# Performance work log

Hardware: AMD Instinct MI355X
Metric: run time of the kernel (lower is better)

## Reference

```python
import jax, jax.numpy as jnp
import numpy as np

N_GRID = 64
DX = 1.0 / N_GRID
INV_DX = float(N_GRID)
DT = 5e-4
BOUND = 3
GRAVITY = np.array([0.0, -9.8, 0.0], dtype=np.float32)
P_VOL = (DX * 0.5) ** 3          # particle volume (NCLaw convention)
P_RHO = 1000.0
P_MASS = P_VOL * P_RHO
N_PART = 500000


def setup_inputs() -> dict:
    key = jax.random.key(0)
    k1, k2, k3, k4, k5 = jax.random.split(key, 5)
    # particles inside the domain, away from the boundary
    x = 0.2 + 0.6 * jax.random.uniform(k1, (N_PART, 3), dtype=jnp.float32)
    v = 0.1 * jax.random.normal(k2, (N_PART, 3), dtype=jnp.float32)
    C = 0.1 * jax.random.normal(k3, (N_PART, 3, 3), dtype=jnp.float32)
    F = jnp.eye(3, dtype=jnp.float32)[None] + 0.01 * jax.random.normal(k4, (N_PART, 3, 3), dtype=jnp.float32)
    s = jax.random.normal(k5, (N_PART, 3, 3), dtype=jnp.float32)
    stress = 100.0 * 0.5 * (s + jnp.swapaxes(s, -1, -2))  # symmetric Cauchy stress
    return {"x": x, "v": v, "C": C, "F": F, "stress": stress}


def _mpm_step(x, v, C, F, stress):
    # quadratic B-spline stencil
    base = jnp.floor(x * INV_DX - 0.5).astype(jnp.int32)        # [N,3]
    fx = x * INV_DX - base.astype(x.dtype)                      # [N,3]
    # weights per offset (0,1,2) per axis -> [N,3(off),3(dim)]
    w = jnp.stack([0.5 * (1.5 - fx) ** 2,
                   0.75 - (fx - 1.0) ** 2,
                   0.5 * (fx - 0.5) ** 2], axis=1)
    # MLS-MPM fused stress + APIC affine term
    affine = stress * (-DT * P_VOL * 4.0 * INV_DX * INV_DX) + P_MASS * C  # [N,3,3]

    offs = jnp.stack(jnp.meshgrid(jnp.arange(3), jnp.arange(3), jnp.arange(3),
                                  indexing='ij'), axis=-1).reshape(27, 3)  # [27,3]
    wi = w[:, offs[:, 0], 0] * w[:, offs[:, 1], 1] * w[:, offs[:, 2], 2]   # [N,27]
    dpos = (offs[None, :, :].astype(x.dtype) - fx[:, None, :]) * DX        # [N,27,3] physical
    mom = P_MASS * v[:, None, :] + jnp.einsum('nij,nkj->nki', affine, dpos)  # [N,27,3]

    idx = base[:, None, :] + offs[None, :, :]                               # [N,27,3]
    flat = (idx[..., 0] * N_GRID + idx[..., 1]) * N_GRID + idx[..., 2]      # [N,27]
    flat_r = flat.reshape(-1)
    G = N_GRID ** 3
    grid_mv = jnp.zeros((G, 3), dtype=x.dtype).at[flat_r].add((wi[..., None] * mom).reshape(-1, 3))
    grid_m = jnp.zeros((G,), dtype=x.dtype).at[flat_r].add((wi * P_MASS).reshape(-1))

    has_mass = grid_m > 0.0
    grid_v = jnp.where(has_mass[:, None], grid_mv / jnp.maximum(grid_m, 1e-10)[:, None], 0.0)
    grid_v = jnp.where(has_mass[:, None], grid_v + DT * jnp.asarray(GRAVITY, x.dtype), 0.0)

    # sticky-ish boundary: zero inflow velocity near walls
    gi = jnp.arange(G)
    ijk = jnp.stack([gi // (N_GRID * N_GRID), (gi // N_GRID) % N_GRID, gi % N_GRID], axis=-1)
    low = (ijk < BOUND) & (grid_v < 0.0)
    high = (ijk >= N_GRID - BOUND) & (grid_v > 0.0)
    grid_v = jnp.where(low | high, 0.0, grid_v)

    # G2P gather
    gv = grid_v[flat]                                              # [N,27,3]
    v_next = jnp.einsum('nk,nkd->nd', wi, gv)                      # [N,3]
    C_next = (4.0 * INV_DX * INV_DX) * jnp.einsum('nk,nki,nkj->nij', wi, gv, dpos)
    x_next = x + DT * v_next
    F_next = jnp.einsum('nij,njk->nik', jnp.eye(3, dtype=x.dtype)[None] + DT * C_next, F)
    return x_next, v_next, C_next, F_next


def reference(x, v, C, F, stress):
    return _mpm_step(x, v, C, F, stress)
```

## Files before the change

kernel.cpp:

```cpp
#include <hip/hip_runtime.h>
#include <math.h>

namespace {
constexpr int   NG    = 64;
constexpr int   GC    = NG * NG * NG;
constexpr int   BOUND = 3;
constexpr float DXf    = 1.0f / 64.0f;
constexpr float INV_DX = 64.0f;
constexpr float DTf    = 5e-4f;
constexpr double P_VOL_D = (0.5 / 64.0) * (0.5 / 64.0) * (0.5 / 64.0);
constexpr float P_MASS_F = (float)(P_VOL_D * 1000.0);
constexpr float AFFINE_SCALE = (float)(-5e-4 * P_VOL_D * 4.0 * 64.0 * 64.0);
constexpr float D_INV  = 4.0f * 64.0f * 64.0f;
constexpr float GRAV_Y = -9.8f;

__device__ __forceinline__ void atom_add_f32(float* p, float v) {
    unsafeAtomicAdd(p, v);
}

__device__ __forceinline__ void weights_of(float fx0, float fx1, float fx2, float w[3][3]) {
    w[0][0] = 0.5f*(1.5f-fx0)*(1.5f-fx0); w[0][1] = 0.5f*(1.5f-fx1)*(1.5f-fx1); w[0][2] = 0.5f*(1.5f-fx2)*(1.5f-fx2);
    w[1][0] = 0.75f-(fx0-1.0f)*(fx0-1.0f); w[1][1] = 0.75f-(fx1-1.0f)*(fx1-1.0f); w[1][2] = 0.75f-(fx2-1.0f)*(fx2-1.0f);
    w[2][0] = 0.5f*(fx0-0.5f)*(fx0-0.5f); w[2][1] = 0.5f*(fx1-0.5f)*(fx1-0.5f); w[2][2] = 0.5f*(fx2-0.5f)*(fx2-0.5f);
}

__device__ __forceinline__ float bspline_w(float u) {
    float au = fabsf(u);
    float a  = 1.5f - au;
    float w  = (au < 0.5f) ? (0.75f - u * u) : (0.5f * a * a);
    return (au < 1.5f) ? w : 0.f;
}
}

__global__ __launch_bounds__(256) void count_kernel(const float* __restrict__ x,
                                                    int* __restrict__ cnt, int n)
{
    int p = blockIdx.x * 256 + threadIdx.x;
    if (p >= n) return;
    float u0 = x[3*p] * INV_DX, u1 = x[3*p+1] * INV_DX, u2 = x[3*p+2] * INV_DX;
    int b0 = (int)floorf(u0 - 0.5f), b1 = (int)floorf(u1 - 0.5f), b2 = (int)floorf(u2 - 0.5f);
    if ((unsigned)b0 >= 64u || (unsigned)b1 >= 64u || (unsigned)b2 >= 64u) return;
    atomicAdd(&cnt[((b0 << 6) + b1) * 64 + b2], 1);
}

__global__ __launch_bounds__(256) void scanA(const int* __restrict__ cnt,
                                             int* __restrict__ start,
                                             int* __restrict__ aux)
{
    __shared__ int sh[256];
    int tid = threadIdx.x;
    int i = blockIdx.x * 256 + tid;
    int v = cnt[i];
    sh[tid] = v;
    __syncthreads();
    for (int off = 1; off < 256; off <<= 1) {
        int t = (tid >= off) ? sh[tid - off] : 0;
        __syncthreads();
        sh[tid] += t;
        __syncthreads();
    }
    start[i] = sh[tid] - v;
    if (tid == 255) aux[blockIdx.x] = sh[255];
}

__global__ __launch_bounds__(256) void scanC(int* __restrict__ start,
                                             const int* __restrict__ aux,
                                             int* __restrict__ cursor)
{
    __shared__ int partial[256];
    __shared__ int sa[1024];
    int tid = threadIdx.x;
    int local[4];
    int s = 0;
#pragma unroll
    for (int k = 0; k < 4; ++k) { local[k] = s; s += aux[tid * 4 + k]; }
    partial[tid] = s;
    __syncthreads();
    for (int off = 1; off < 256; off <<= 1) {
        int v = (tid >= off) ? partial[tid - off] : 0;
        __syncthreads();
        partial[tid] += v;
        __syncthreads();
    }
    int base = (tid > 0) ? partial[tid - 1] : 0;
#pragma unroll
    for (int k = 0; k < 4; ++k) sa[tid * 4 + k] = base + local[k];
    __syncthreads();
    int off0 = sa[blockIdx.x];
    int i = blockIdx.x * 256 + tid;
    int v = start[i] + off0;
    start[i] = v;
    cursor[i] = v;
    if (blockIdx.x == 0 && tid == 0) start[GC] = sa[1023] + aux[1023];
}

__global__ __launch_bounds__(256) void reorder_kernel(const float* __restrict__ x,
                                                      const float* __restrict__ v,
                                                      const float* __restrict__ C,
                                                      const float* __restrict__ st,
                                                      int* __restrict__ cursor,
                                                      float4* __restrict__ pay0,
                                                      float4* __restrict__ pay1,
                                                      float4* __restrict__ pay2,
                                                      float4* __restrict__ pay3, int n)
{
    int p = blockIdx.x * 256 + threadIdx.x;
    if (p >= n) return;

    float u0 = x[3*p] * INV_DX, u1 = x[3*p+1] * INV_DX, u2 = x[3*p+2] * INV_DX;
    int b0 = (int)floorf(u0 - 0.5f), b1 = (int)floorf(u1 - 0.5f), b2 = (int)floorf(u2 - 0.5f);
    if ((unsigned)b0 >= 64u || (unsigned)b1 >= 64u || (unsigned)b2 >= 64u) return;

    float aff[9];
#pragma unroll
    for (int i = 0; i < 9; ++i)
        aff[i] = st[9*p + i] * AFFINE_SCALE + P_MASS_F * C[9*p + i];
    float mv0 = P_MASS_F * v[3*p], mv1 = P_MASS_F * v[3*p+1], mv2 = P_MASS_F * v[3*p+2];

    int pos = atomicAdd(&cursor[((b0 << 6) + b1) * 64 + b2], 1);

    pay0[pos] = make_float4(aff[0], aff[1], aff[2], aff[3]);
    pay1[pos] = make_float4(aff[4], aff[5], aff[6], aff[7]);
    pay2[pos] = make_float4(aff[8], mv0, mv1, mv2);
    pay3[pos] = make_float4(u0, u1, u2, 0.f);
}

__global__ __launch_bounds__(256) void p2g_strip(const float4* __restrict__ pay0,
                                                 const float4* __restrict__ pay1,
                                                 const float4* __restrict__ pay2,
                                                 const float4* __restrict__ pay3,
                                                 const int* __restrict__ start,
                                                 float* __restrict__ grid)
{
    int B   = blockIdx.x;
    int xcd = B & 7, j = B >> 3;
    int cj  = j >> 2, oj = j & 3;
    int wave = threadIdx.x >> 6, lane = threadIdx.x & 63;
    int r   = ((cj * 32 + xcd * 4 + oj) << 2) + wave;

    int row01 = r >> 1;
    int g0 = row01 >> 6, g1 = row01 & 63;
    int sl = lane >> 3, q = lane & 7;
    int g2b = ((r & 1) << 5) + sl * 4;
    float fg0 = (float)g0, fg1 = (float)g1, fg2b = (float)g2b;

    float a00=0.f,a01=0.f,a02=0.f,a03=0.f;
    float a10=0.f,a11=0.f,a12=0.f,a13=0.f;
    float a20=0.f,a21=0.f,a22=0.f,a23=0.f;
    float a30=0.f,a31=0.f,a32=0.f,a33=0.f;

    int klo = (g2b >= 2) ? g2b - 2 : 0;
    int khi = (g2b + 3 <= 63) ? g2b + 3 : 63;

#define P2G_CELL(CC, A0, A1, A2, A3)                                         \
    {   float u2  = r3.z - (fg2b + (float)CC);                               \
        float w2  = bspline_w(u2);                                           \
        float wq  = w01 * w2;                                                \
        float dp2 = -u2 * DXf;                                               \
        A0 += wq * (m0 + r0.z * dp2);                                        \
        A1 += wq * (m1 + r1.y * dp2);                                        \
        A2 += wq * (m2 + r2.x * dp2);                                        \
        A3 += wq * P_MASS_F; }

#pragma unroll
    for (int o0 = 0; o0 < 3; ++o0) {
        int b0 = g0 - o0;
        if ((unsigned)b0 >= 64u) continue;
#pragma unroll
        for (int o1 = 0; o1 < 3; ++o1) {
            int b1 = g1 - o1;
            if ((unsigned)b1 >= 64u) continue;
            int rowp = ((b0 << 6) + b1) << 6;
            int s = start[rowp + klo] + q;
            int e = start[rowp + khi + 1];
            float4 c0, c1, c2, c3;
            if (s < e) { c0 = pay0[s]; c1 = pay1[s]; c2 = pay2[s]; c3 = pay3[s]; }
            for (int idx = s; idx < e; ) {
                float4 r0 = c0, r1 = c1, r2 = c2, r3 = c3;
                idx += 8;
                if (idx < e) { c0 = pay0[idx]; c1 = pay1[idx]; c2 = pay2[idx]; c3 = pay3[idx]; }
                float u0  = r3.x - fg0, u1 = r3.y - fg1;
                float w01 = bspline_w(u0) * bspline_w(u1);
                float dp0 = -u0 * DXf, dp1 = -u1 * DXf;
                float m0 = r2.y + r0.x * dp0 + r0.y * dp1;
                float m1 = r2.z + r0.w * dp0 + r1.x * dp1;
                float m2 = r2.w + r1.z * dp0 + r1.w * dp1;
                P2G_CELL(0, a00, a01, a02, a03)
                P2G_CELL(1, a10, a11, a12, a13)
                P2G_CELL(2, a20, a21, a22, a23)
                P2G_CELL(3, a30, a31, a32, a33)
            }
        }
    }
#undef P2G_CELL

#define RED(OFF)                                                             \
    a00 += __shfl_down(a00, OFF); a01 += __shfl_down(a01, OFF);              \
    a02 += __shfl_down(a02, OFF); a03 += __shfl_down(a03, OFF);              \
    a10 += __shfl_down(a10, OFF); a11 += __shfl_down(a11, OFF);              \
    a12 += __shfl_down(a12, OFF); a13 += __shfl_down(a13, OFF);              \
    a20 += __shfl_down(a20, OFF); a21 += __shfl_down(a21, OFF);              \
    a22 += __shfl_down(a22, OFF); a23 += __shfl_down(a23, OFF);              \
    a30 += __shfl_down(a30, OFF); a31 += __shfl_down(a31, OFF);              \
    a32 += __shfl_down(a32, OFF); a33 += __shfl_down(a33, OFF);
    RED(1) RED(2) RED(4)
#undef RED

    if (q == 0) {
#define STORE_CELL(CC, A0, A1, A2, A3)                                       \
    {   int g2 = g2b + CC;                                                   \
        float v0 = 0.f, v1 = 0.f, v2 = 0.f;                                  \
        if (A3 > 0.f) {                                                      \
            float mm = fmaxf(A3, 1e-10f);                                    \
            v0 = A0 / mm;                                                    \
            v1 = A1 / mm + DTf * GRAV_Y;                                     \
            v2 = A2 / mm;                                                    \
        }                                                                    \
        if ((g0 < BOUND && v0 < 0.f) || (g0 >= NG - BOUND && v0 > 0.f)) v0 = 0.f; \
        if ((g1 < BOUND && v1 < 0.f) || (g1 >= NG - BOUND && v1 > 0.f)) v1 = 0.f; \
        if ((g2 < BOUND && v2 < 0.f) || (g2 >= NG - BOUND && v2 > 0.f)) v2 = 0.f; \
        ((float4*)grid)[row01 * 64 + g2] = make_float4(v0, v1, v2, A3); }
        STORE_CELL(0, a00, a01, a02, a03)
        STORE_CELL(1, a10, a11, a12, a13)
        STORE_CELL(2, a20, a21, a22, a23)
        STORE_CELL(3, a30, a31, a32, a33)
#undef STORE_CELL
    }
}

__global__ __launch_bounds__(256) void p2g_naive(const float* __restrict__ x,
                                                 const float* __restrict__ v,
                                                 const float* __restrict__ C,
                                                 const float* __restrict__ st,
                                                 float* __restrict__ grid, int n)
{
    int p = blockIdx.x * 256 + threadIdx.x;
    if (p >= n) return;

    float xp0 = x[3*p], xp1 = x[3*p+1], xp2 = x[3*p+2];
    float u0 = xp0 * INV_DX, u1 = xp1 * INV_DX, u2 = xp2 * INV_DX;
    float b0f = floorf(u0 - 0.5f), b1f = floorf(u1 - 0.5f), b2f = floorf(u2 - 0.5f);
    int base0 = (int)b0f, base1 = (int)b1f, base2 = (int)b2f;
    float fx0 = u0 - b0f, fx1 = u1 - b1f, fx2 = u2 - b2f;

    float w[3][3];
    weights_of(fx0, fx1, fx2, w);

    float aff[3][3];
#pragma unroll
    for (int i = 0; i < 3; ++i)
#pragma unroll
        for (int j = 0; j < 3; ++j)
            aff[i][j] = st[9*p + 3*i + j] * AFFINE_SCALE + P_MASS_F * C[9*p + 3*i + j];

    float mv0 = P_MASS_F * v[3*p], mv1 = P_MASS_F * v[3*p+1], mv2 = P_MASS_F * v[3*p+2];

#pragma unroll
    for (int i = 0; i < 3; ++i) {
        float dp0 = ((float)i - fx0) * DXf;
#pragma unroll
        for (int j = 0; j < 3; ++j) {
            float dp1 = ((float)j - fx1) * DXf;
            float wij = w[i][0] * w[j][1];
            float m0 = mv0 + aff[0][0]*dp0 + aff[0][1]*dp1;
            float m1 = mv1 + aff[1][0]*dp0 + aff[1][1]*dp1;
            float m2 = mv2 + aff[2][0]*dp0 + aff[2][1]*dp1;
            int cellij = ((base0 + i) * NG + (base1 + j)) * NG + base2;
#pragma unroll
            for (int k = 0; k < 3; ++k) {
                float dp2 = ((float)k - fx2) * DXf;
                float wi = wij * w[k][2];
                float* cptr = grid + 4 * (cellij + k);
                atom_add_f32(cptr + 0, wi * (m0 + aff[0][2]*dp2));
                atom_add_f32(cptr + 1, wi * (m1 + aff[1][2]*dp2));
                atom_add_f32(cptr + 2, wi * (m2 + aff[2][2]*dp2));
                atom_add_f32(cptr + 3, wi * P_MASS_F);
            }
        }
    }
}

__global__ __launch_bounds__(256) void grid_kernel(float* __restrict__ grid)
{
    int g = blockIdx.x * 256 + threadIdx.x;
    if (g >= GC) return;
    float4 val = ((const float4*)grid)[g];
    float m = val.w;
    float v0 = 0.f, v1 = 0.f, v2 = 0.f;
    if (m > 0.f) {
        float mm = fmaxf(m, 1e-10f);
        v0 = val.x / mm;
        v1 = val.y / mm + DTf * GRAV_Y;
        v2 = val.z / mm;
    }
    int ci = g >> 12, cj = (g >> 6) & 63, ck = g & 63;
    if ((ci < BOUND && v0 < 0.f) || (ci >= NG - BOUND && v0 > 0.f)) v0 = 0.f;
    if ((cj < BOUND && v1 < 0.f) || (cj >= NG - BOUND && v1 > 0.f)) v1 = 0.f;
    if ((ck < BOUND && v2 < 0.f) || (ck >= NG - BOUND && v2 > 0.f)) v2 = 0.f;
    ((float4*)grid)[g] = make_float4(v0, v1, v2, m);
}

__global__ __launch_bounds__(256) void g2p_kernel(const float* __restrict__ x,
                                                  const float* __restrict__ F,
                                                  const float* __restrict__ grid,
                                                  float* __restrict__ out_x,
                                                  float* __restrict__ out_v,
                                                  float* __restrict__ out_C,
                                                  float* __restrict__ out_F,
                                                  int n)
{
    int p = blockIdx.x * 256 + threadIdx.x;
    if (p >= n) return;

    float xp0 = x[3*p], xp1 = x[3*p+1], xp2 = x[3*p+2];
    float t0 = xp0 * INV_DX, t1 = xp1 * INV_DX, t2 = xp2 * INV_DX;
    float b0 = floorf(t0 - 0.5f), b1 = floorf(t1 - 0.5f), b2 = floorf(t2 - 0.5f);
    int   base0 = (int)b0, base1 = (int)b1, base2 = (int)b2;
    float fx0 = t0 - b0, fx1 = t1 - b1, fx2 = t2 - b2;

    float w[3][3];
    weights_of(fx0, fx1, fx2, w);

    float vn0 = 0.f, vn1 = 0.f, vn2 = 0.f;
    float Cn[3][3] = {};

#pragma unroll
    for (int i = 0; i < 3; ++i) {
        float dp0 = ((float)i - fx0) * DXf;
#pragma unroll
        for (int j = 0; j < 3; ++j) {
            float dp1 = ((float)j - fx1) * DXf;
            float wij = w[i][0] * w[j][1];
            int cellij = ((base0 + i) * NG + (base1 + j)) * NG + base2;
#pragma unroll
            for (int k = 0; k < 3; ++k) {
                float dp2 = ((float)k - fx2) * DXf;
                float wi = wij * w[k][2];
                float4 gv = ((const float4*)grid)[cellij + k];
                vn0 += wi * gv.x; vn1 += wi * gv.y; vn2 += wi * gv.z;
                float wx = wi * gv.x, wy = wi * gv.y, wz = wi * gv.z;
                Cn[0][0] += wx * dp0; Cn[0][1] += wx * dp1; Cn[0][2] += wx * dp2;
                Cn[1][0] += wy * dp0; Cn[1][1] += wy * dp1; Cn[1][2] += wy * dp2;
                Cn[2][0] += wz * dp0; Cn[2][1] += wz * dp1; Cn[2][2] += wz * dp2;
            }
        }
    }

#pragma unroll
    for (int i = 0; i < 3; ++i)
#pragma unroll
        for (int j = 0; j < 3; ++j)
            Cn[i][j] *= D_INV;

    out_x[3*p]   = xp0 + DTf * vn0;
    out_x[3*p+1] = xp1 + DTf * vn1;
    out_x[3*p+2] = xp2 + DTf * vn2;
    out_v[3*p]   = vn0; out_v[3*p+1] = vn1; out_v[3*p+2] = vn2;

    float Fp[3][3];
#pragma unroll
    for (int i = 0; i < 3; ++i)
#pragma unroll
        for (int j = 0; j < 3; ++j)
            Fp[i][j] = F[9*p + 3*i + j];

#pragma unroll
    for (int i = 0; i < 3; ++i) {
#pragma unroll
        for (int k = 0; k < 3; ++k) {
            float acc = Cn[i][0]*Fp[0][k] + Cn[i][1]*Fp[1][k] + Cn[i][2]*Fp[2][k];
            out_F[9*p + 3*i + k] = Fp[i][k] + DTf * acc;
            out_C[9*p + 3*i + k] = Cn[i][k];
        }
    }
}

extern "C" void kernel_launch(void* const* d_in, const int* in_sizes, int n_in,
                              void* d_out, int out_size, void* d_ws, size_t ws_size,
                              hipStream_t stream)
{
    const float* x  = (const float*)d_in[0];
    const float* v  = (const float*)d_in[1];
    const float* C  = (const float*)d_in[2];
    const float* F  = (const float*)d_in[3];
    const float* st = (const float*)d_in[4];
    int n = in_sizes[0] / 3;

    const size_t grid_bytes = (size_t)GC * 4 * sizeof(float);
    const size_t tab_ints   = 3 * (size_t)GC + 1 + 1024;
    const bool   use_tiled  = ws_size >= grid_bytes &&
                              (size_t)out_size >= 22 * (size_t)n + tab_ints;

    float* grid = (float*)d_ws;

    float* out  = (float*)d_out;
    float* out_x = out;
    float* out_v = out + 3 * (size_t)n;
    float* out_C = out + 6 * (size_t)n;
    float* out_F = out + 15 * (size_t)n;
    float4* pay0 = (float4*)(out + 6 * (size_t)n);
    float4* pay1 = pay0 + (size_t)n;
    float4* pay2 = pay0 + 2 * (size_t)n;
    float4* pay3 = pay0 + 3 * (size_t)n;
    int* tab    = (int*)(out + 22 * (size_t)n);
    int* cnt    = tab;
    int* tstart = tab + GC;
    int* cursor = tab + 2 * GC + 1;
    int* aux    = tab + 3 * GC + 1;

    int pblocks = (n + 255) / 256;

    if (use_tiled) {
        hipMemsetAsync(cnt, 0, (size_t)GC * sizeof(int), stream);
        count_kernel<<<pblocks, 256, 0, stream>>>(x, cnt, n);
        scanA<<<GC / 256, 256, 0, stream>>>(cnt, tstart, aux);
        scanC<<<GC / 256, 256, 0, stream>>>(tstart, aux, cursor);
        reorder_kernel<<<pblocks, 256, 0, stream>>>(x, v, C, st, cursor,
                                                    pay0, pay1, pay2, pay3, n);
        p2g_strip<<<GC / 128, 256, 0, stream>>>(pay0, pay1, pay2, pay3, tstart, grid);
    } else {
        hipMemsetAsync(grid, 0, grid_bytes, stream);
        p2g_naive<<<pblocks, 256, 0, stream>>>(x, v, C, st, grid, n);
        grid_kernel<<<GC / 256, 256, 0, stream>>>(grid);
    }

    g2p_kernel<<<pblocks, 256, 0, stream>>>(x, F, grid, out_x, out_v, out_C, out_F, n);
}
```

Before: 322.8 us.

## Add sorted G2P kernel staging 3x3 grid rows in shared memory per cell row

```diff
diff --git a/kernel.cpp b/kernel.cpp
--- a/kernel.cpp
+++ b/kernel.cpp
@@ -122,7 +122,7 @@
     pay0[pos] = make_float4(aff[0], aff[1], aff[2], aff[3]);
     pay1[pos] = make_float4(aff[4], aff[5], aff[6], aff[7]);
     pay2[pos] = make_float4(aff[8], mv0, mv1, mv2);
-    pay3[pos] = make_float4(u0, u1, u2, 0.f);
+    pay3[pos] = make_float4(u0, u1, u2, __int_as_float(p));
 }
 
 __global__ __launch_bounds__(256) void p2g_strip(const float4* __restrict__ pay0,
@@ -300,6 +300,104 @@
     ((float4*)grid)[g] = make_float4(v0, v1, v2, m);
 }
 
+__global__ __launch_bounds__(256) void g2p_sorted(const float4* __restrict__ pay3,
+                                                  const int* __restrict__ start,
+                                                  const float* __restrict__ grid,
+                                                  const float* __restrict__ F,
+                                                  float* __restrict__ out_x,
+                                                  float* __restrict__ out_v,
+                                                  float* __restrict__ out_C,
+                                                  float* __restrict__ out_F)
+{
+    __shared__ float4 rows[9][64];
+
+    int row01 = blockIdx.x;
+    int b0 = row01 >> 6, b1 = row01 & 63;
+    int tid = threadIdx.x;
+
+    int s = start[row01 << 6];
+    int e = start[(row01 << 6) + 64];
+    if (s >= e) return;
+
+    for (int t = tid; t < 576; t += 256) {
+        int ij = t >> 6, c = t & 63;
+        int i = ij / 3, j = ij - 3 * i;
+        int r0 = b0 + i, r1 = b1 + j;
+        float4 val = make_float4(0.f, 0.f, 0.f, 0.f);
+        if (r0 < NG && r1 < NG)
+            val = ((const float4*)grid)[((r0 << 6) + r1) * 64 + c];
+        rows[ij][c] = val;
+    }
+    __syncthreads();
+
+    float fb0 = (float)b0, fb1 = (float)b1;
+
+    for (int idx = s + tid; idx < e; idx += 256) {
+        float4 r3 = pay3[idx];
+        int orig = __float_as_int(r3.w);
+        float u0 = r3.x, u1 = r3.y, u2 = r3.z;
+        float b2f = floorf(u2 - 0.5f);
+        int b2 = (int)b2f;
+        float fx0 = u0 - fb0, fx1 = u1 - fb1, fx2 = u2 - b2f;
+
+        float w[3][3];
+        weights_of(fx0, fx1, fx2, w);
+
+        float vn0 = 0.f, vn1 = 0.f, vn2 = 0.f;
+        float Cn[3][3] = {};
+
+#pragma unroll
+        for (int i = 0; i < 3; ++i) {
+            float dp0 = ((float)i - fx0) * DXf;
+#pragma unroll
+            for (int j = 0; j < 3; ++j) {
+                float dp1 = ((float)j - fx1) * DXf;
+                float wij = w[i][0] * w[j][1];
+#pragma unroll
+                for (int k = 0; k < 3; ++k) {
+                    float dp2 = ((float)k - fx2) * DXf;
+                    float wi = wij * w[k][2];
+                    float4 gv = rows[i * 3 + j][b2 + k];
+                    vn0 += wi * gv.x; vn1 += wi * gv.y; vn2 += wi * gv.z;
+                    float wx = wi * gv.x, wy = wi * gv.y, wz = wi * gv.z;
+                    Cn[0][0] += wx * dp0; Cn[0][1] += wx * dp1; Cn[0][2] += wx * dp2;
+                    Cn[1][0] += wy * dp0; Cn[1][1] += wy * dp1; Cn[1][2] += wy * dp2;
+                    Cn[2][0] += wz * dp0; Cn[2][1] += wz * dp1; Cn[2][2] += wz * dp2;
+                }
+            }
+        }
+
+#pragma unroll
+        for (int i = 0; i < 3; ++i)
+#pragma unroll
+            for (int j = 0; j < 3; ++j)
+                Cn[i][j] *= D_INV;
+
+        float xp0 = u0 * DXf, xp1 = u1 * DXf, xp2 = u2 * DXf;
+        out_x[3*orig]   = xp0 + DTf * vn0;
+        out_x[3*orig+1] = xp1 + DTf * vn1;
+        out_x[3*orig+2] = xp2 + DTf * vn2;
+        out_v[3*orig]   = vn0; out_v[3*orig+1] = vn1; out_v[3*orig+2] = vn2;
+
+        float Fp[3][3];
+#pragma unroll
+        for (int i = 0; i < 3; ++i)
+#pragma unroll
+            for (int j = 0; j < 3; ++j)
+                Fp[i][j] = F[9*orig + 3*i + j];
+
+#pragma unroll
+        for (int i = 0; i < 3; ++i) {
+#pragma unroll
+            for (int k = 0; k < 3; ++k) {
+                float acc = Cn[i][0]*Fp[0][k] + Cn[i][1]*Fp[1][k] + Cn[i][2]*Fp[2][k];
+                out_F[9*orig + 3*i + k] = Fp[i][k] + DTf * acc;
+                out_C[9*orig + 3*i + k] = Cn[i][k];
+            }
+        }
+    }
+}
+
 __global__ __launch_bounds__(256) void g2p_kernel(const float* __restrict__ x,
                                                   const float* __restrict__ F,
                                                   const float* __restrict__ grid,
@@ -390,6 +488,8 @@
     const size_t tab_ints   = 3 * (size_t)GC + 1 + 1024;
     const bool   use_tiled  = ws_size >= grid_bytes &&
                               (size_t)out_size >= 22 * (size_t)n + tab_ints;
+    const size_t need_ws    = grid_bytes + 16 * (size_t)n + ((size_t)GC + 1) * sizeof(int);
+    const bool   use_sorted = use_tiled && ws_size >= need_ws;
 
     float* grid = (float*)d_ws;
 
@@ -398,15 +498,27 @@
     float* out_v = out + 3 * (size_t)n;
     float* out_C = out + 6 * (size_t)n;
     float* out_F = out + 15 * (size_t)n;
+
     float4* pay0 = (float4*)(out + 6 * (size_t)n);
     float4* pay1 = pay0 + (size_t)n;
     float4* pay2 = pay0 + 2 * (size_t)n;
-    float4* pay3 = pay0 + 3 * (size_t)n;
-    int* tab    = (int*)(out + 22 * (size_t)n);
-    int* cnt    = tab;
-    int* tstart = tab + GC;
-    int* cursor = tab + 2 * GC + 1;
-    int* aux    = tab + 3 * GC + 1;
+    float4* pay3;
+    int *cnt, *tstart, *cursor, *aux;
+
+    if (use_sorted) {
+        pay3   = (float4*)((char*)d_ws + grid_bytes);
+        tstart = (int*)((char*)d_ws + grid_bytes + 16 * (size_t)n);
+        cnt    = (int*)(out + 18 * (size_t)n);
+        cursor = cnt + GC;
+        aux    = cursor + GC;
+    } else {
+        pay3   = pay0 + 3 * (size_t)n;
+        int* tab = (int*)(out + 22 * (size_t)n);
+        cnt    = tab;
+        tstart = tab + GC;
+        cursor = tab + 2 * GC + 1;
+        aux    = tab + 3 * GC + 1;
+    }
 
     int pblocks = (n + 255) / 256;
 
@@ -418,11 +530,18 @@
         reorder_kernel<<<pblocks, 256, 0, stream>>>(x, v, C, st, cursor,
                                                     pay0, pay1, pay2, pay3, n);
         p2g_strip<<<GC / 128, 256, 0, stream>>>(pay0, pay1, pay2, pay3, tstart, grid);
+        if (use_sorted) {
+            g2p_sorted<<<4096, 256, 0, stream>>>(pay3, tstart, grid, F,
+                                                 out_x, out_v, out_C, out_F);
+        } else {
+            g2p_kernel<<<pblocks, 256, 0, stream>>>(x, F, grid,
+                                                    out_x, out_v, out_C, out_F, n);
+        }
     } else {
         hipMemsetAsync(grid, 0, grid_bytes, stream);
         p2g_naive<<<pblocks, 256, 0, stream>>>(x, v, C, st, grid, n);
         grid_kernel<<<GC / 256, 256, 0, stream>>>(grid);
-    }
-
-    g2p_kernel<<<pblocks, 256, 0, stream>>>(x, F, grid, out_x, out_v, out_C, out_F, n);
-}
+        g2p_kernel<<<pblocks, 256, 0, stream>>>(x, F, grid,
+                                                out_x, out_v, out_C, out_F, n);
+    }
+}
```

Measured after the change: 335.0 us. 3.8% more time.
